# Optimization experiments

Hardware: AMD Instinct MI355X
Metric: run time of the kernel (lower is better)

The kernel has to match this reference:

```python
import jax, jax.numpy as jnp
import numpy as np

DIM = 768
N_HEADS = 12
HEAD_DIM = DIM // N_HEADS
SCALE = HEAD_DIM ** -0.5


def setup_inputs() -> dict:
    key = jax.random.key(0)
    kx, kqkv, kpw, kpb = jax.random.split(key, 4)
    B, N = 16, 1024
    x = jax.random.normal(kx, (B, N, DIM), dtype=jnp.float32)
    # nn.Linear weights stored [out, in]; torch computes x @ W.T + b
    w_qkv = jax.random.normal(kqkv, (3 * DIM, DIM), dtype=jnp.float32) * (DIM ** -0.5)
    w_proj = jax.random.normal(kpw, (DIM, DIM), dtype=jnp.float32) * (DIM ** -0.5)
    b_proj = jax.random.normal(kpb, (DIM,), dtype=jnp.float32) * 0.01
    return {"x": x, "w_qkv": w_qkv, "w_proj": w_proj, "b_proj": b_proj}


def reference(x, w_qkv, w_proj, b_proj):
    B, N, C = x.shape
    # qkv: [B, N, 3C] -> [3, B, H, N, Dh]
    qkv = (x @ w_qkv.T).reshape(B, N, 3, N_HEADS, HEAD_DIM)
    qkv = jnp.transpose(qkv, (2, 0, 3, 1, 4))
    q, k, v = qkv[0], qkv[1], qkv[2]
    # scores: [B, H, N, N]
    scores = jnp.einsum("bhnd,bhmd->bhnm", q, k) * SCALE
    attn = jax.nn.softmax(scores, axis=-1)
    out = jnp.einsum("bhnm,bhmd->bhnd", attn, v)
    out = jnp.transpose(out, (0, 2, 1, 3)).reshape(B, N, C)
    return out @ w_proj.T + b_proj
```

## Files before the change

### kernel.cpp

```cpp
#include <hip/hip_runtime.h>
#include <stdint.h>


typedef unsigned short u16;
typedef __attribute__((ext_vector_type(8))) short s16x8;
typedef __attribute__((ext_vector_type(4))) float f32x4;
typedef __attribute__((ext_vector_type(4))) unsigned short u16x4;

#define SEQ 1024
#define NHEAD 12
#define HD 64

__device__ __forceinline__ u16 f2bf(float f) {
  union { float f; uint32_t u; } v; v.f = f;
  uint32_t u = v.u;
  return (u16)((u + 0x7FFFu + ((u >> 16) & 1u)) >> 16);
}

__device__ __forceinline__ float exp2_fast(float x) {
  return __builtin_amdgcn_exp2f(x);
}

__device__ __forceinline__ uint32_t pk_bf16(float a, float b) {
#if __has_builtin(__builtin_amdgcn_cvt_pk_bf16_f32)
  typedef __attribute__((ext_vector_type(2))) __bf16 bf2;
  union { bf2 v; uint32_t u; } c;
  c.v = __builtin_amdgcn_cvt_pk_bf16_f32(a, b);
  return c.u;
#else
  union { float f; uint32_t u; } ua, ub; ua.f = a; ub.f = b;
  const uint32_t ra = ua.u + 0x8000u, rb = ub.u + 0x8000u;
  return __builtin_amdgcn_perm(ra, rb, 0x03020706u);
#endif
}

__device__ __forceinline__ void gld_lds16(const void* g, void* l) {
  __builtin_amdgcn_global_load_lds((const __attribute__((address_space(1))) void*)g,
                                   (__attribute__((address_space(3))) void*)l, 16, 0, 0);
}

__global__ void cvt_bf16_3(const float* __restrict__ in0, u16* __restrict__ out0, int n0,
                           const float* __restrict__ in1, u16* __restrict__ out1, int n1,
                           const float* __restrict__ in2, u16* __restrict__ out2, int n2) {
  int i = blockIdx.x * blockDim.x + threadIdx.x;
  const float* in; u16* out;
  if (i < n0)            { in = in0; out = out0; }
  else if (i < n0 + n1)  { in = in1; out = out1; i -= n0; }
  else if (i < n0 + n1 + n2) { in = in2; out = out2; i -= n0 + n1; }
  else return;
  float4 f = ((const float4*)in)[i];
  u16x4 o;
  o.x = f2bf(f.x); o.y = f2bf(f.y); o.z = f2bf(f.z); o.w = f2bf(f.w);
  ((u16x4*)out)[i] = o;
}

template <int EPI>
__global__ __launch_bounds__(256, 3)
void gemm_bt(const u16* __restrict__ A, const u16* __restrict__ B,
             u16* __restrict__ q, u16* __restrict__ k, u16* __restrict__ v,
             float* __restrict__ out, const float* __restrict__ bias) {
  __shared__ u16 As[128 * 64];
  __shared__ u16 Bs[128 * 64];
  const int tid = threadIdx.x;
  const int wv = tid >> 6, lane = tid & 63;
  const int quad = lane >> 4, l16 = lane & 15;
  const int m0 = blockIdx.x * 128, n0 = blockIdx.y * 128;
  const int wm = (wv & 1) * 64, wn = (wv >> 1) * 64;

  f32x4 acc[4][4];
#pragma unroll
  for (int i = 0; i < 4; i++)
#pragma unroll
    for (int j = 0; j < 4; j++) { acc[i][j].x = 0.f; acc[i][j].y = 0.f; acc[i][j].z = 0.f; acc[i][j].w = 0.f; }

  const int srow = (lane >> 3);
  const int scp = lane & 7;

  for (int kt = 0; kt < 768; kt += 64) {
    __syncthreads();
#pragma unroll
    for (int i = 0; i < 4; i++) {
      const int t = wv * 4 + i;
      const int row = t * 8 + srow;
      const int c = scp ^ (row & 7);
      gld_lds16(A + (size_t)(m0 + row) * 768 + kt + c * 8, &As[t * 512]);
      gld_lds16(B + (size_t)(n0 + row) * 768 + kt + c * 8, &Bs[t * 512]);
    }
    __syncthreads();
#pragma unroll
    for (int ks = 0; ks < 2; ks++) {
      s16x8 af[4], bf[4];
#pragma unroll
      for (int mi = 0; mi < 4; mi++) {
        const int ra = wm + mi * 16 + l16;
        const int ca = ((ks * 4 + quad) ^ (ra & 7)) * 8;
        af[mi] = *(const s16x8*)&As[ra * 64 + ca];
        const int rb = wn + mi * 16 + l16;
        const int cb = ((ks * 4 + quad) ^ (rb & 7)) * 8;
        bf[mi] = *(const s16x8*)&Bs[rb * 64 + cb];
      }
#pragma unroll
      for (int mi = 0; mi < 4; mi++)
#pragma unroll
        for (int ni = 0; ni < 4; ni++)
          acc[mi][ni] = __builtin_amdgcn_mfma_f32_16x16x32_bf16(af[mi], bf[ni], acc[mi][ni], 0, 0, 0);
    }
  }

#pragma unroll
  for (int mi = 0; mi < 4; mi++) {
#pragma unroll
    for (int ni = 0; ni < 4; ni++) {
#pragma unroll
      for (int r = 0; r < 4; r++) {
        const int m = m0 + wm + mi * 16 + quad * 4 + r;
        const int n = n0 + wn + ni * 16 + l16;
        const float val = acc[mi][ni][r];
        if (EPI == 0) {
          const int which = n / 768;
          const int rc = n % 768;
          const int head = rc >> 6, d = rc & 63;
          const int b = m >> 10, rr = m & 1023;
          if (which == 0)
            q[((size_t)(b * NHEAD + head) * SEQ + rr) * HD + d] = f2bf(val * 0.18033688011112042f);
          else if (which == 1)
            k[((size_t)(b * NHEAD + head) * SEQ + rr) * HD + d] = f2bf(val);
          else
            v[((size_t)(b * NHEAD + head) * HD + d) * SEQ + rr] = f2bf(val);
        } else {
          out[(size_t)m * 768 + n] = val + bias[n];
        }
      }
    }
  }
}

__global__ __launch_bounds__(256, 3)
void flash_attn(const u16* __restrict__ Q, const u16* __restrict__ K,
                const u16* __restrict__ VT, u16* __restrict__ O) {
  __shared__ u16 Ks[2][64 * 64];
  __shared__ u16 Vs[2][64 * 64];
  __shared__ u16 Ps[4][32 * 64];

  const int tid = threadIdx.x;
  const int wv = tid >> 6, lane = tid & 63;
  const int quad = lane >> 4, l16 = lane & 15;
  const int bh = blockIdx.x;
  const int q0 = blockIdx.y * 128 + wv * 32;
  const size_t base = (size_t)bh * SEQ * HD;
  const size_t vbase = (size_t)bh * HD * SEQ;
  u16* pw = Ps[wv];

  const int sr0 = tid >> 3;
  const int sc0 = (tid & 7) ^ (sr0 & 7);
  const int sr1 = 32 + sr0;
  const int sc1 = (tid & 7) ^ (sr1 & 7);

  s16x8 qf[2][2];
#pragma unroll
  for (int g = 0; g < 2; g++)
#pragma unroll
    for (int ks = 0; ks < 2; ks++)
      qf[g][ks] = *(const s16x8*)(Q + base + (size_t)(q0 + g * 16 + l16) * HD + ks * 32 + quad * 8);

  const s16x8 ones = {0x3F80, 0x3F80, 0x3F80, 0x3F80, 0x3F80, 0x3F80, 0x3F80, 0x3F80};

  f32x4 acc[2][4], acc_l[2];
#pragma unroll
  for (int g = 0; g < 2; g++) {
    acc_l[g].x = 0.f; acc_l[g].y = 0.f; acc_l[g].z = 0.f; acc_l[g].w = 0.f;
#pragma unroll
    for (int t = 0; t < 4; t++) { acc[g][t].x = 0.f; acc[g][t].y = 0.f; acc[g][t].z = 0.f; acc[g][t].w = 0.f; }
  }

  const int swz = l16 & 7;

  gld_lds16(K + base + (size_t)sr0 * HD + sc0 * 8, &Ks[0][wv * 512]);
  gld_lds16(VT + vbase + (size_t)sr0 * SEQ + sc0 * 8, &Vs[0][wv * 512]);
  gld_lds16(K + base + (size_t)sr1 * HD + sc1 * 8, &Ks[0][2048 + wv * 512]);
  gld_lds16(VT + vbase + (size_t)sr1 * SEQ + sc1 * 8, &Vs[0][2048 + wv * 512]);

  for (int it = 0; it < 16; it++) {
    __syncthreads();
    if (it + 1 < 16) {
      const int n1 = (it + 1) * 64;
      const int nb = (it + 1) & 1;
      gld_lds16(K + base + (size_t)(n1 + sr0) * HD + sc0 * 8, &Ks[nb][wv * 512]);
      gld_lds16(VT + vbase + (size_t)sr0 * SEQ + n1 + sc0 * 8, &Vs[nb][wv * 512]);
      gld_lds16(K + base + (size_t)(n1 + sr1) * HD + sc1 * 8, &Ks[nb][2048 + wv * 512]);
      gld_lds16(VT + vbase + (size_t)sr1 * SEQ + n1 + sc1 * 8, &Vs[nb][2048 + wv * 512]);
    }
    const u16* __restrict__ ks = Ks[it & 1];
    const u16* __restrict__ vs = Vs[it & 1];

    f32x4 s0[4], s1[4];
    __builtin_amdgcn_s_setprio(1);
#pragma unroll
    for (int t = 0; t < 4; t++) {
      s0[t].x = 0.f; s0[t].y = 0.f; s0[t].z = 0.f; s0[t].w = 0.f;
      s1[t].x = 0.f; s1[t].y = 0.f; s1[t].z = 0.f; s1[t].w = 0.f;
      const u16* kr = &ks[(t * 16 + l16) * 64];
      const s16x8 kf0 = *(const s16x8*)&kr[(quad ^ swz) * 8];
      const s16x8 kf1 = *(const s16x8*)&kr[((4 + quad) ^ swz) * 8];
      s0[t] = __builtin_amdgcn_mfma_f32_16x16x32_bf16(kf0, qf[0][0], s0[t], 0, 0, 0);
      s0[t] = __builtin_amdgcn_mfma_f32_16x16x32_bf16(kf1, qf[0][1], s0[t], 0, 0, 0);
      s1[t] = __builtin_amdgcn_mfma_f32_16x16x32_bf16(kf0, qf[1][0], s1[t], 0, 0, 0);
      s1[t] = __builtin_amdgcn_mfma_f32_16x16x32_bf16(kf1, qf[1][1], s1[t], 0, 0, 0);
    }
    __builtin_amdgcn_s_setprio(0);

#pragma unroll
    for (int t = 0; t < 4; t++)
#pragma unroll
      for (int r = 0; r < 4; r++) {
        s0[t][r] = exp2_fast(s0[t][r]);
        s1[t][r] = exp2_fast(s1[t][r]);
      }

#pragma unroll
    for (int t = 0; t < 4; t++) {
      const int p = (2 * t + (quad >> 1)) ^ swz;
      *(uint2*)&pw[l16 * 64 + p * 8 + (quad & 1) * 4] =
          make_uint2(pk_bf16(s0[t][0], s0[t][1]), pk_bf16(s0[t][2], s0[t][3]));
      *(uint2*)&pw[(16 + l16) * 64 + p * 8 + (quad & 1) * 4] =
          make_uint2(pk_bf16(s1[t][0], s1[t][1]), pk_bf16(s1[t][2], s1[t][3]));
    }

    __builtin_amdgcn_s_setprio(1);
#pragma unroll
    for (int ks2 = 0; ks2 < 2; ks2++) {
      const int cp = ((ks2 * 4 + quad) ^ swz) * 8;
      const s16x8 pf0 = *(const s16x8*)&pw[l16 * 64 + cp];
      const s16x8 pf1 = *(const s16x8*)&pw[(16 + l16) * 64 + cp];
      acc_l[0] = __builtin_amdgcn_mfma_f32_16x16x32_bf16(pf0, ones, acc_l[0], 0, 0, 0);
      acc_l[1] = __builtin_amdgcn_mfma_f32_16x16x32_bf16(pf1, ones, acc_l[1], 0, 0, 0);
#pragma unroll
      for (int t2 = 0; t2 < 4; t2++) {
        const s16x8 vf = *(const s16x8*)&vs[(t2 * 16 + l16) * 64 + cp];
        acc[0][t2] = __builtin_amdgcn_mfma_f32_16x16x32_bf16(pf0, vf, acc[0][t2], 0, 0, 0);
        acc[1][t2] = __builtin_amdgcn_mfma_f32_16x16x32_bf16(pf1, vf, acc[1][t2], 0, 0, 0);
      }
    }
    __builtin_amdgcn_s_setprio(0);
  }

  const int b = bh / NHEAD, h = bh % NHEAD;
#pragma unroll
  for (int g = 0; g < 2; g++) {
#pragma unroll
    for (int r = 0; r < 4; r++) {
      const float li = 1.0f / acc_l[g][r];
      const int qrow = q0 + g * 16 + quad * 4 + r;
      u16* op = O + (size_t)(b * SEQ + qrow) * 768 + h * HD;
#pragma unroll
      for (int t2 = 0; t2 < 4; t2++)
        op[t2 * 16 + l16] = f2bf(acc[g][t2][r] * li);
    }
  }
}

extern "C" void kernel_launch(void* const* d_in, const int* in_sizes, int n_in,
                              void* d_out, int out_size, void* d_ws, size_t ws_size,
                              hipStream_t stream) {
  (void)in_sizes; (void)n_in; (void)out_size; (void)ws_size;
  const float* x      = (const float*)d_in[0];
  const float* w_qkv  = (const float*)d_in[1];
  const float* w_proj = (const float*)d_in[2];
  const float* b_proj = (const float*)d_in[3];

  const size_t SZ_X   = (size_t)16384 * 768;
  const size_t SZ_WQ  = (size_t)2304 * 768;
  const size_t SZ_WP  = (size_t)768 * 768;
  const size_t SZ_HED = (size_t)16 * NHEAD * SEQ * HD;

  u16* xb   = (u16*)d_ws;
  u16* wqb  = xb + SZ_X;
  u16* wpb  = wqb + SZ_WQ;
  u16* qb   = wpb + SZ_WP;
  u16* kb   = qb + SZ_HED;
  u16* vtb  = kb + SZ_HED;
  u16* attn = vtb + SZ_HED;

  const int n0 = (int)(SZ_X / 4), n1 = (int)(SZ_WQ / 4), n2 = (int)(SZ_WP / 4);
  const int nblk = (n0 + n1 + n2 + 255) / 256;
  cvt_bf16_3<<<nblk, 256, 0, stream>>>(x, xb, n0, w_qkv, wqb, n1, w_proj, wpb, n2);

  gemm_bt<0><<<dim3(128, 18), 256, 0, stream>>>(xb, wqb, qb, kb, vtb, nullptr, nullptr);
  flash_attn<<<dim3(192, 8), 256, 0, stream>>>(qb, kb, vtb, attn);
  gemm_bt<1><<<dim3(128, 6), 256, 0, stream>>>(attn, wpb, nullptr, nullptr, nullptr,
                                               (float*)d_out, b_proj);
}
```

Before: 282.0 us.

## Keep P in registers by permuting V columns in QKV epilogue

The flash attention kernel no longer sends the exponentiated scores through shared memory. The MFMA output fragments are packed straight into A-operand registers, which works because the QKV GEMM epilogue now writes V^T with its sequence index permuted to match the register layout of those fragments. The V epilogue also switches to vectorized 4-element stores, and dropping the P buffer frees LDS. The cost is a tight coupling between the V permutation and the MFMA lane layout: if the two disagree, the output is silently wrong.

```diff
diff --git a/kernel.cpp b/kernel.cpp
--- a/kernel.cpp
+++ b/kernel.cpp
@@ -107,31 +107,51 @@
     }
   }
 
-#pragma unroll
-  for (int mi = 0; mi < 4; mi++) {
+  if (EPI == 0) {
 #pragma unroll
     for (int ni = 0; ni < 4; ni++) {
-#pragma unroll
-      for (int r = 0; r < 4; r++) {
-        const int m = m0 + wm + mi * 16 + quad * 4 + r;
-        const int n = n0 + wn + ni * 16 + l16;
-        const float val = acc[mi][ni][r];
-        if (EPI == 0) {
-          const int which = n / 768;
-          const int rc = n % 768;
-          const int head = rc >> 6, d = rc & 63;
-          const int b = m >> 10, rr = m & 1023;
-          if (which == 0)
-            q[((size_t)(b * NHEAD + head) * SEQ + rr) * HD + d] = f2bf(val * 0.18033688011112042f);
-          else if (which == 1)
-            k[((size_t)(b * NHEAD + head) * SEQ + rr) * HD + d] = f2bf(val);
-          else
-            v[((size_t)(b * NHEAD + head) * HD + d) * SEQ + rr] = f2bf(val);
-        } else {
-          out[(size_t)m * 768 + n] = val + bias[n];
+      const int n = n0 + wn + ni * 16 + l16;
+      const int which = n / 768;
+      const int rc = n % 768;
+      const int head = rc >> 6, d = rc & 63;
+      if (which == 2) {
+#pragma unroll
+        for (int mi = 0; mi < 4; mi++) {
+          const int mb = m0 + wm + mi * 16 + quad * 4;
+          const int b = mb >> 10, rrb = mb & 1023;
+          const int vcol = (rrb & ~31) | (((rrb >> 2) & 3) << 3) | (((rrb >> 4) & 1) << 2);
+          u16x4 pk4;
+          pk4.x = f2bf(acc[mi][ni][0]); pk4.y = f2bf(acc[mi][ni][1]);
+          pk4.z = f2bf(acc[mi][ni][2]); pk4.w = f2bf(acc[mi][ni][3]);
+          *(u16x4*)&v[((size_t)(b * NHEAD + head) * HD + d) * SEQ + vcol] = pk4;
+        }
+      } else {
+#pragma unroll
+        for (int mi = 0; mi < 4; mi++) {
+#pragma unroll
+          for (int r = 0; r < 4; r++) {
+            const int m = m0 + wm + mi * 16 + quad * 4 + r;
+            const int b = m >> 10, rr = m & 1023;
+            const float val = acc[mi][ni][r];
+            if (which == 0)
+              q[((size_t)(b * NHEAD + head) * SEQ + rr) * HD + d] = f2bf(val * 0.18033688011112042f);
+            else
+              k[((size_t)(b * NHEAD + head) * SEQ + rr) * HD + d] = f2bf(val);
+          }
         }
       }
     }
+  } else {
+#pragma unroll
+    for (int mi = 0; mi < 4; mi++)
+#pragma unroll
+      for (int ni = 0; ni < 4; ni++)
+#pragma unroll
+        for (int r = 0; r < 4; r++) {
+          const int m = m0 + wm + mi * 16 + quad * 4 + r;
+          const int n = n0 + wn + ni * 16 + l16;
+          out[(size_t)m * 768 + n] = acc[mi][ni][r] + bias[n];
+        }
   }
 }
 
@@ -140,7 +160,6 @@
                 const u16* __restrict__ VT, u16* __restrict__ O) {
   __shared__ u16 Ks[2][64 * 64];
   __shared__ u16 Vs[2][64 * 64];
-  __shared__ u16 Ps[4][32 * 64];
 
   const int tid = threadIdx.x;
   const int wv = tid >> 6, lane = tid & 63;
@@ -149,7 +168,6 @@
   const int q0 = blockIdx.y * 128 + wv * 32;
   const size_t base = (size_t)bh * SEQ * HD;
   const size_t vbase = (size_t)bh * HD * SEQ;
-  u16* pw = Ps[wv];
 
   const int sr0 = tid >> 3;
   const int sc0 = (tid & 7) ^ (sr0 & 7);
@@ -217,28 +235,26 @@
         s1[t][r] = exp2_fast(s1[t][r]);
       }
 
-#pragma unroll
-    for (int t = 0; t < 4; t++) {
-      const int p = (2 * t + (quad >> 1)) ^ swz;
-      *(uint2*)&pw[l16 * 64 + p * 8 + (quad & 1) * 4] =
-          make_uint2(pk_bf16(s0[t][0], s0[t][1]), pk_bf16(s0[t][2], s0[t][3]));
-      *(uint2*)&pw[(16 + l16) * 64 + p * 8 + (quad & 1) * 4] =
-          make_uint2(pk_bf16(s1[t][0], s1[t][1]), pk_bf16(s1[t][2], s1[t][3]));
-    }
-
     __builtin_amdgcn_s_setprio(1);
 #pragma unroll
     for (int ks2 = 0; ks2 < 2; ks2++) {
+      union { uint32_t w[4]; s16x8 v; } pa0, pa1;
+      pa0.w[0] = pk_bf16(s0[2 * ks2][0], s0[2 * ks2][1]);
+      pa0.w[1] = pk_bf16(s0[2 * ks2][2], s0[2 * ks2][3]);
+      pa0.w[2] = pk_bf16(s0[2 * ks2 + 1][0], s0[2 * ks2 + 1][1]);
+      pa0.w[3] = pk_bf16(s0[2 * ks2 + 1][2], s0[2 * ks2 + 1][3]);
+      pa1.w[0] = pk_bf16(s1[2 * ks2][0], s1[2 * ks2][1]);
+      pa1.w[1] = pk_bf16(s1[2 * ks2][2], s1[2 * ks2][3]);
+      pa1.w[2] = pk_bf16(s1[2 * ks2 + 1][0], s1[2 * ks2 + 1][1]);
+      pa1.w[3] = pk_bf16(s1[2 * ks2 + 1][2], s1[2 * ks2 + 1][3]);
+      acc_l[0] = __builtin_amdgcn_mfma_f32_16x16x32_bf16(pa0.v, ones, acc_l[0], 0, 0, 0);
+      acc_l[1] = __builtin_amdgcn_mfma_f32_16x16x32_bf16(pa1.v, ones, acc_l[1], 0, 0, 0);
       const int cp = ((ks2 * 4 + quad) ^ swz) * 8;
-      const s16x8 pf0 = *(const s16x8*)&pw[l16 * 64 + cp];
-      const s16x8 pf1 = *(const s16x8*)&pw[(16 + l16) * 64 + cp];
-      acc_l[0] = __builtin_amdgcn_mfma_f32_16x16x32_bf16(pf0, ones, acc_l[0], 0, 0, 0);
-      acc_l[1] = __builtin_amdgcn_mfma_f32_16x16x32_bf16(pf1, ones, acc_l[1], 0, 0, 0);
 #pragma unroll
       for (int t2 = 0; t2 < 4; t2++) {
         const s16x8 vf = *(const s16x8*)&vs[(t2 * 16 + l16) * 64 + cp];
-        acc[0][t2] = __builtin_amdgcn_mfma_f32_16x16x32_bf16(pf0, vf, acc[0][t2], 0, 0, 0);
-        acc[1][t2] = __builtin_amdgcn_mfma_f32_16x16x32_bf16(pf1, vf, acc[1][t2], 0, 0, 0);
+        acc[0][t2] = __builtin_amdgcn_mfma_f32_16x16x32_bf16(pa0.v, vf, acc[0][t2], 0, 0, 0);
+        acc[1][t2] = __builtin_amdgcn_mfma_f32_16x16x32_bf16(pa1.v, vf, acc[1][t2], 0, 0, 0);
       }
     }
     __builtin_amdgcn_s_setprio(0);
```

After: 261.7 us. 7.2% less time.
